# Performance work log

Measured on AMD Instinct MI355X. Metric: run time of the kernel, lower is better.

Reference implementation:

```python
import jax, jax.numpy as jnp
import numpy as np

B, NUM_CLASSES, H, W, CF = 2, 19, 64, 64, 256
TOPK_IDX = 20  # hard-coded in the torch source: sorted descending value at index 20


def _cosine(x):
    # x: [B, N, D] -> clamped cosine affinity [B, N, N]
    xn = x / (jnp.linalg.norm(x, axis=2, keepdims=True) + 1e-9)
    return jnp.maximum(jnp.einsum('bnd,bmd->bnm', xn, xn), 0.0)


def _conv1x1(x, w, b):
    # x: [B, C, H, W], w: [O, C], b: [O]
    return jnp.einsum('bchw,oc->bohw', x, w) + b[None, :, None, None]


def setup_inputs() -> dict:
    key = jax.random.key(0)
    ks = jax.random.split(key, 12)
    s_c = (2.0 / NUM_CLASSES) ** 0.5  # kaiming fan_in scale for 1x1 conv
    s_f = (2.0 / CF) ** 0.5
    return {
        'pred': jax.random.normal(ks[0], (B, NUM_CLASSES, H, W), jnp.float32),
        'feat': jax.random.normal(ks[1], (B, CF, H, W), jnp.float32),
        'w_cls1': jax.random.normal(ks[2], (NUM_CLASSES, NUM_CLASSES), jnp.float32) * s_c,
        'b_cls1': jnp.zeros((NUM_CLASSES,), jnp.float32),
        'w_cls2': jax.random.normal(ks[3], (NUM_CLASSES, NUM_CLASSES), jnp.float32) * s_c,
        'b_cls2': jnp.zeros((NUM_CLASSES,), jnp.float32),
        'w_pro1': jax.random.normal(ks[4], (CF, CF), jnp.float32) * s_f,
        'b_pro1': jnp.zeros((CF,), jnp.float32),
        'w_pro2': jax.random.normal(ks[5], (CF, CF), jnp.float32) * s_f,
        'b_pro2': jnp.zeros((CF,), jnp.float32),
        'class_weight': jnp.ones((NUM_CLASSES,), jnp.float32),
    }


def reference(pred, feat, w_cls1, b_cls1, w_cls2, b_cls2,
              w_pro1, b_pro1, w_pro2, b_pro2, class_weight):
    bsz, c, h, w = feat.shape
    C = pred.shape[1]
    N = h * w
    feat_flat = feat.reshape(bsz, c, N).transpose(0, 2, 1)  # [B, N, 256]

    # --- no_grad block 1: confidence mask + top-k sparsified cosine affinity ---
    prob = jax.nn.softmax(pred, axis=1)
    p_prob = prob.max(axis=1)      # [B, H, W]
    p_max = prob.argmax(axis=1)    # [B, H, W]
    cwm = class_weight / (class_weight.max() + 1e-10) * 0.95
    mask = ((p_prob >= 0.95) | (p_prob >= cwm[p_max])).astype(jnp.float32)
    mask = jax.lax.stop_gradient(mask.reshape(bsz, N, 1))  # broadcast over classes

    aff1 = _cosine(feat_flat)                                # [B, N, N]
    thr = -jnp.sort(-aff1, axis=-1)[:, :, TOPK_IDX:TOPK_IDX + 1]  # per-row 21st largest
    aff1 = jnp.where(aff1 < thr, 0.0, aff1)
    aff1 = jax.lax.stop_gradient(aff1 + aff1.transpose(0, 2, 1))

    # --- degree-normalized propagation of predictions ---
    pred_flat = pred.reshape(bsz, C, N).transpose(0, 2, 1)   # [B, N, C]
    d1 = (aff1.sum(-1) + 1e-10) ** -0.5                      # D^{-1/2}
    aff1n = d1[:, :, None] * aff1 * d1[:, None, :]           # D^{-1/2} A D^{-1/2}
    p2 = jnp.einsum('bnm,bmc->bnc', aff1n, pred_flat)
    p3 = (0.8 * p2 + 0.2 * pred_flat) * (1.0 - mask) + (0.2 * p2 + 0.8 * pred_flat) * mask
    pred2 = p3.transpose(0, 2, 1).reshape(bsz, C, h, w)
    pred_out = _conv1x1(_conv1x1(pred2, w_cls1, b_cls1), w_cls2, b_cls2)

    # --- no_grad block 2: class-consistency-masked affinity over refined softmax ---
    oh = jax.nn.one_hot(p_max, C, dtype=jnp.float32)         # [B, H, W, C]
    # faithful to torch: permute(0,2,3,1) on the already-[B,H,W,C] one-hot, then flat view
    oh = jnp.transpose(oh, (0, 2, 3, 1)).reshape(bsz, -1, C)
    sp = jax.nn.softmax(pred_out, axis=1).reshape(bsz, C, N).transpose(0, 2, 1)
    aff_f = _cosine(sp)
    aff_f = jnp.where(_cosine(oh) == 0.0, 0.0, aff_f)
    d2 = (aff_f.sum(-1) + 1e-10) ** -0.5
    aff_fn = jax.lax.stop_gradient(d2[:, :, None] * aff_f * d2[:, None, :])

    # --- propagate features and project ---
    new_feat = jnp.einsum('bnm,bmc->bnc', aff_fn, feat_flat)
    new_feat = new_feat.transpose(0, 2, 1).reshape(bsz, c, h, w)
    feat_out = _conv1x1(jax.nn.relu(_conv1x1(new_feat, w_pro1, b_pro1)), w_pro2, b_pro2)
    return pred_out, feat_out
```

## Files before the change

kernel.cpp:

```cpp
#include <hip/hip_runtime.h>

#define NN 4096
#define DD 256
#define CC 19
#define BB 2
#define KSPLIT 4

typedef __attribute__((ext_vector_type(8))) short bf16x8;
typedef _Float16 f16x8 __attribute__((ext_vector_type(8)));
typedef __attribute__((ext_vector_type(4))) float f32x4;

#define GLL16(gp, lp) __builtin_amdgcn_global_load_lds( \
    (const __attribute__((address_space(1))) unsigned int*)(gp), \
    (__attribute__((address_space(3))) unsigned int*)(lp), 16, 0, 0)

__device__ inline unsigned short f2b(float f) {
  unsigned int u = __float_as_uint(f);
  return (unsigned short)((u + 0x7FFFu + ((u >> 16) & 1u)) >> 16);
}
__device__ inline float b2f(unsigned short h) {
  return __uint_as_float(((unsigned int)h) << 16);
}
__device__ inline unsigned int pack2(float a, float b) {
  return (unsigned int)f2b(a) | ((unsigned int)f2b(b) << 16);
}
__device__ inline void split16(float x, unsigned short& h, unsigned short& l) {
  _Float16 hh = (_Float16)x;
  float hf = (float)hh;
  _Float16 ll = (_Float16)((x - hf) * 2048.0f);
  h = *reinterpret_cast<unsigned short*>(&hh);
  l = *reinterpret_cast<unsigned short*>(&ll);
}

__global__ void k_mask_bits(const float* __restrict__ pred, const float* __restrict__ cw,
                            float* __restrict__ maskb, unsigned int* __restrict__ ohbits) {
  int g = blockIdx.x * 256 + threadIdx.x;
  if (g >= BB * NN) return;
  int b = g >> 12, n = g & (NN - 1);
  const float* p = pred + (size_t)b * CC * NN + n;
  float v[CC];
  float mx = -1e30f; int am = 0;
#pragma unroll
  for (int c = 0; c < CC; ++c) {
    float t = p[(size_t)c * NN];
    v[c] = t;
    if (t > mx) { mx = t; am = c; }
  }
  float s = 0.f;
#pragma unroll
  for (int c = 0; c < CC; ++c) s += expf(v[c] - mx);
  float pprob = 1.f / s;
  float cmax = 0.f;
#pragma unroll
  for (int c = 0; c < CC; ++c) cmax = fmaxf(cmax, cw[c]);
  float cwm = cw[am] / (cmax + 1e-10f) * 0.95f;
  maskb[g] = (pprob >= 0.95f || pprob >= cwm) ? 1.f : 0.f;
  int h = n >> 6, w = n & 63;
  int L = w * (CC * 64) + am * 64 + h;
  atomicOr(&ohbits[b * NN + L / CC], 1u << (L % CC));
}

__global__ void k_norm_feat(const float* __restrict__ feat,
                            unsigned short* __restrict__ xh, unsigned short* __restrict__ xl) {
  int g = blockIdx.x * 64 + threadIdx.x;
  int b = g >> 12, n = g & (NN - 1);
  const float* f = feat + (size_t)b * DD * NN + n;
  float s = 0.f;
  for (int d = 0; d < DD; ++d) { float t = f[(size_t)d * NN]; s += t * t; }
  float r = 1.f / (sqrtf(s) + 1e-9f);
  size_t ob = ((size_t)b * NN + n) * DD;
  for (int d = 0; d < DD; d += 4) {
    ushort4 oh, ol;
    split16(f[(size_t)d * NN] * r, oh.x, ol.x);
    split16(f[(size_t)(d + 1) * NN] * r, oh.y, ol.y);
    split16(f[(size_t)(d + 2) * NN] * r, oh.z, ol.z);
    split16(f[(size_t)(d + 3) * NN] * r, oh.w, ol.w);
    *reinterpret_cast<ushort4*>(&xh[ob + d]) = oh;
    *reinterpret_cast<ushort4*>(&xl[ob + d]) = ol;
  }
}

__global__ __launch_bounds__(256, 2) void k_gram1(const unsigned short* __restrict__ xh,
                                                  const unsigned short* __restrict__ xl,
                                                  float* __restrict__ M) {
  int L = blockIdx.x;
  int b = blockIdx.y;
  int I = 0;
  while (L >= 32 - I) { L -= 32 - I; ++I; }
  int J = I + L;
  int i0 = I * 128, j0 = J * 128;
  float* Mb = M + (size_t)b * NN * NN;
  const unsigned short* XH = xh + (size_t)b * NN * DD;
  const unsigned short* XL = xl + (size_t)b * NN * DD;
  __shared__ unsigned short stage[2][4][128][32];
  int t = threadIdx.x;
  int wave = t >> 6, lane = t & 63;
  int wr = (wave & 1) * 64, wc = (wave >> 1) * 64;
  int lrow = lane & 15, quad = lane >> 4;
  int sel = (lrow >> 1) & 3;
  f32x4 accH[4][4] = {}, accL[4][4] = {};
  const unsigned short* src = (wave == 0) ? XH + (size_t)i0 * DD
                             : (wave == 1) ? XL + (size_t)i0 * DD
                             : (wave == 2) ? XH + (size_t)j0 * DD
                                           : XL + (size_t)j0 * DD;
  int srow = lane >> 2;
  int spart = (lane & 3) ^ ((lane >> 3) & 3);
#pragma unroll
  for (int e = 0; e < 8; ++e)
    GLL16(&src[(size_t)(e * 16 + srow) * DD + spart * 8], &stage[0][wave][e * 16][0]);
  __syncthreads();
  int cur = 0;
  for (int k0 = 0; k0 < DD; k0 += 32) {
    if (k0 + 32 < DD) {
#pragma unroll
      for (int e = 0; e < 8; ++e)
        GLL16(&src[(size_t)(e * 16 + srow) * DD + k0 + 32 + spart * 8],
              &stage[cur ^ 1][wave][e * 16][0]);
    }
    f16x8 ah[4], al[4], bh[4], bl[4];
#pragma unroll
    for (int i = 0; i < 4; ++i) {
      int ra = wr + i * 16 + lrow;
      int rb = wc + i * 16 + lrow;
      int sl = (quad ^ sel) * 8;
      ah[i] = *reinterpret_cast<const f16x8*>(&stage[cur][0][ra][sl]);
      al[i] = *reinterpret_cast<const f16x8*>(&stage[cur][1][ra][sl]);
      bh[i] = *reinterpret_cast<const f16x8*>(&stage[cur][2][rb][sl]);
      bl[i] = *reinterpret_cast<const f16x8*>(&stage[cur][3][rb][sl]);
    }
#pragma unroll
    for (int i = 0; i < 4; ++i) {
#pragma unroll
      for (int j = 0; j < 4; ++j) {
        accH[i][j] = __builtin_amdgcn_mfma_f32_16x16x32_f16(ah[i], bh[j], accH[i][j], 0, 0, 0);
        accL[i][j] = __builtin_amdgcn_mfma_f32_16x16x32_f16(ah[i], bl[j], accL[i][j], 0, 0, 0);
        accL[i][j] = __builtin_amdgcn_mfma_f32_16x16x32_f16(al[i], bh[j], accL[i][j], 0, 0, 0);
      }
    }
    __syncthreads();
    cur ^= 1;
  }
#pragma unroll
  for (int i = 0; i < 4; ++i)
#pragma unroll
    for (int j = 0; j < 4; ++j)
#pragma unroll
      for (int reg = 0; reg < 4; ++reg)
        accH[i][j][reg] = fmaxf(accH[i][j][reg] + accL[i][j][reg] * 4.8828125e-4f, 0.f);
  float* buf = (float*)stage;
  int rr = t >> 4, cc = t & 15;
  for (int half = 0; half < 2; ++half) {
    __syncthreads();
    if ((wr >> 6) == half) {
#pragma unroll
      for (int i = 0; i < 4; ++i)
#pragma unroll
        for (int j = 0; j < 4; ++j)
#pragma unroll
          for (int reg = 0; reg < 4; ++reg)
            buf[(i * 16 + quad * 4 + reg) * 132 + wc + j * 16 + lrow] = accH[i][j][reg];
    }
    __syncthreads();
#pragma unroll
    for (int i = 0; i < 4; ++i) {
      int row = rr + i * 16;
#pragma unroll
      for (int q = 0; q < 2; ++q) {
        int col = cc * 4 + q * 64;
        *reinterpret_cast<float4*>(&Mb[(size_t)(i0 + half * 64 + row) * NN + j0 + col]) =
            *reinterpret_cast<float4*>(&buf[row * 132 + col]);
      }
    }
  }
  if (I != J) {
    for (int half = 0; half < 2; ++half) {
      __syncthreads();
      if ((wc >> 6) == half) {
#pragma unroll
        for (int i = 0; i < 4; ++i)
#pragma unroll
          for (int j = 0; j < 4; ++j)
#pragma unroll
            for (int reg = 0; reg < 4; ++reg)
              buf[(j * 16 + lrow) * 132 + wr + i * 16 + quad * 4 + reg] = accH[i][j][reg];
      }
      __syncthreads();
#pragma unroll
      for (int i = 0; i < 4; ++i) {
        int row = rr + i * 16;
#pragma unroll
        for (int q = 0; q < 2; ++q) {
          int col = cc * 4 + q * 64;
          *reinterpret_cast<float4*>(&Mb[(size_t)(j0 + half * 64 + row) * NN + i0 + col]) =
              *reinterpret_cast<float4*>(&buf[row * 132 + col]);
        }
      }
    }
  }
}

__global__ __launch_bounds__(256, 2) void k_topk(const float* __restrict__ M,
                                                 float* __restrict__ thr) {
  __shared__ unsigned int cbuf[4][64];
  int b = blockIdx.y;
  int wave = threadIdx.x >> 6, lane = threadIdx.x & 63;
  int n = blockIdx.x * 4 + wave;
  const float* row = M + (size_t)b * NN * NN + (size_t)n * NN;
  uint4 v[16];
#pragma unroll
  for (int e = 0; e < 16; ++e) {
    unsigned long long addr = (unsigned long long)(row + lane * 4 + e * 256);
    asm volatile("global_load_dwordx4 %0, %1, off" : "=v"(v[e]) : "v"(addr));
  }
  asm volatile("s_waitcnt vmcnt(0)" ::: "memory");
  __builtin_amdgcn_sched_barrier(0);
  unsigned int mx = 0u;
#pragma unroll
  for (int e = 0; e < 16; ++e) {
    unsigned int a = v[e].x > v[e].y ? v[e].x : v[e].y;
    unsigned int c2 = v[e].z > v[e].w ? v[e].z : v[e].w;
    a = a > c2 ? a : c2;
    mx = mx > a ? mx : a;
  }
  unsigned int lo = 0u, hi = 0x3FC00000u;
  while (lo < hi) {
    unsigned int mid = lo + ((hi - lo + 1) >> 1);
    if (__popcll(__ballot(mx >= mid)) >= 21) lo = mid; else hi = mid - 1;
  }
  unsigned int s = lo;
  unsigned int base = 0;
  unsigned long long ltmask = (1ull << lane) - 1ull;
#pragma unroll
  for (int e = 0; e < 16; ++e) {
#pragma unroll
    for (int q = 0; q < 4; ++q) {
      unsigned int val = (q == 0) ? v[e].x : (q == 1) ? v[e].y : (q == 2) ? v[e].z : v[e].w;
      unsigned long long mk = __ballot(val >= s);
      if (mk) {
        unsigned int pos = base + (unsigned int)__popcll(mk & ltmask);
        if (val >= s && pos < 64u) cbuf[wave][pos] = val;
        base += (unsigned int)__popcll(mk);
      }
    }
  }
  asm volatile("s_waitcnt lgkmcnt(0)" ::: "memory");
  __builtin_amdgcn_sched_barrier(0);
  unsigned int t = s;
  if (base <= 64u) {
    unsigned int cand = (lane < (int)base) ? cbuf[wave][lane] : 0u;
    lo = s; hi = 0x3FC00000u;
    while (lo < hi) {
      unsigned int mid = lo + ((hi - lo + 1) >> 1);
      if (__popcll(__ballot(cand >= mid)) >= 21) lo = mid; else hi = mid - 1;
    }
    t = lo;
  }
  {
    unsigned int t1 = t + 1u;
    int c1 = 0, c2 = 0;
#pragma unroll
    for (int e = 0; e < 16; ++e) {
      c1 += (int)__popcll(__ballot(v[e].x >= t));
      c1 += (int)__popcll(__ballot(v[e].y >= t));
      c1 += (int)__popcll(__ballot(v[e].z >= t));
      c1 += (int)__popcll(__ballot(v[e].w >= t));
      c2 += (int)__popcll(__ballot(v[e].x >= t1));
      c2 += (int)__popcll(__ballot(v[e].y >= t1));
      c2 += (int)__popcll(__ballot(v[e].z >= t1));
      c2 += (int)__popcll(__ballot(v[e].w >= t1));
    }
    if (!(c1 >= 21 && c2 < 21)) {
      lo = 0u; hi = 0x40000000u;
      while (lo < hi) {
        unsigned int mid = lo + ((hi - lo + 1) >> 1);
        int c = 0;
#pragma unroll
        for (int e = 0; e < 16; ++e) {
          c += (int)__popcll(__ballot(v[e].x >= mid));
          c += (int)__popcll(__ballot(v[e].y >= mid));
          c += (int)__popcll(__ballot(v[e].z >= mid));
          c += (int)__popcll(__ballot(v[e].w >= mid));
        }
        if (c >= 21) lo = mid; else hi = mid - 1;
      }
      t = lo;
    }
  }
  if (lane == 0) thr[b * NN + n] = __uint_as_float(t);
}

__global__ __launch_bounds__(256) void k_symm(float* __restrict__ M, const float* __restrict__ thr,
                                              float* __restrict__ dsum) {
  int L = blockIdx.x;
  int b = blockIdx.y;
  int I = 0;
  while (L >= 64 - I) { L -= 64 - I; ++I; }
  int J = I + L;
  float* Mb = M + (size_t)b * NN * NN;
  unsigned short* Mus = (unsigned short*)Mb;
  const float* th = thr + b * NN;
  __shared__ float A[64][65];
  int t = threadIdx.x;
  int i0 = I * 64, j0 = J * 64;
  float areg[16];
#pragma unroll
  for (int e = 0; e < 16; ++e) {
    int lin = t + e * 256;
    int i = lin >> 6, j = lin & 63;
    areg[e] = Mb[(size_t)(i0 + i) * NN + j0 + j];
  }
#pragma unroll
  for (int e = 0; e < 16; ++e) {
    int lin = t + e * 256;
    int i = lin >> 6, j = lin & 63;
    float a = areg[e];
    float v = a * ((a >= th[i0 + i] ? 1.f : 0.f) + (a >= th[j0 + j] ? 1.f : 0.f));
    A[i][j] = v;
  }
  __syncthreads();
  {
    int i = t >> 2, seg = (t & 3) * 16;
    float v[16];
#pragma unroll
    for (int q = 0; q < 4; ++q)
      *reinterpret_cast<float4*>(&v[q * 4]) = *reinterpret_cast<float4*>(&A[i][seg + q * 4]);
    unsigned int pk[8];
#pragma unroll
    for (int q = 0; q < 8; ++q) pk[q] = pack2(v[2 * q], v[2 * q + 1]);
    size_t ub = 2 * (size_t)(i0 + i) * NN + 2 * (size_t)j0 + seg;
    *reinterpret_cast<int4*>(&Mus[ub])     = *reinterpret_cast<int4*>(&pk[0]);
    *reinterpret_cast<int4*>(&Mus[ub + 8]) = *reinterpret_cast<int4*>(&pk[4]);
  }
  if (I != J) {
    int j = t >> 2, seg = (t & 3) * 16;
    float v[16];
#pragma unroll
    for (int e = 0; e < 16; ++e) v[e] = A[seg + e][j];
    unsigned int pk[8];
#pragma unroll
    for (int q = 0; q < 8; ++q) pk[q] = pack2(v[2 * q], v[2 * q + 1]);
    size_t ub = 2 * (size_t)(j0 + j) * NN + 2 * (size_t)i0 + seg;
    *reinterpret_cast<int4*>(&Mus[ub])     = *reinterpret_cast<int4*>(&pk[0]);
    *reinterpret_cast<int4*>(&Mus[ub + 8]) = *reinterpret_cast<int4*>(&pk[4]);
  }
  if (t < 64) {
    float s = 0.f;
#pragma unroll
    for (int j = 0; j < 64; ++j) s += A[t][j];
    atomicAdd(&dsum[b * NN + i0 + t], s);
  } else if (t < 128 && I != J) {
    int j = t - 64;
    float s = 0.f;
#pragma unroll
    for (int i = 0; i < 64; ++i) s += A[i][j];
    atomicAdd(&dsum[b * NN + j0 + j], s);
  }
}

__global__ void k_fin_d(float* __restrict__ d) {
  int g = blockIdx.x * 256 + threadIdx.x;
  if (g < BB * NN) d[g] = 1.f / sqrtf(d[g] + 1e-10f);
}

__global__ void k_make_yb(const float* __restrict__ pred, const float* __restrict__ d1,
                          unsigned short* __restrict__ ybh) {
  int g = blockIdx.x * 256 + threadIdx.x;
  int idx = g * 4;
  int b = idx / (32 * NN);
  int c = (idx / NN) & 31;
  int n = idx & (NN - 1);
  ushort4 o = make_ushort4(0, 0, 0, 0);
  if (c < CC) {
    float4 p = *reinterpret_cast<const float4*>(&pred[((size_t)b * CC + c) * NN + n]);
    const float* dd = d1 + b * NN + n;
    o.x = f2b(p.x * dd[0]); o.y = f2b(p.y * dd[1]);
    o.z = f2b(p.z * dd[2]); o.w = f2b(p.w * dd[3]);
  }
  *reinterpret_cast<ushort4*>(&ybh[idx]) = o;
}

__global__ __launch_bounds__(256) void k_p2_mfma(
    const float* __restrict__ M, const unsigned short* __restrict__ ybh,
    const float* __restrict__ d1, float* __restrict__ p2b) {
  int b = blockIdx.y;
  int n0 = blockIdx.x * 64;
  const unsigned short* Mus = (const unsigned short*)(M + (size_t)b * NN * NN);
  const unsigned short* Y = ybh + (size_t)b * 32 * NN;
  __shared__ unsigned short As[64][72];
  __shared__ unsigned short Ys[32][72];
  int t = threadIdx.x;
  int wave = t >> 6, lane = t & 63;
  int wn = (wave & 1) * 32;
  int wc = (wave >> 1) * 16;
  int lrow = lane & 15, quad = lane >> 4;
  f32x4 acc[2] = {{0.f,0.f,0.f,0.f},{0.f,0.f,0.f,0.f}};
  int sr = t >> 3, scc = (t & 7) * 8;
  for (int m0 = 0; m0 < NN; m0 += 64) {
#pragma unroll
    for (int e = 0; e < 2; ++e) {
      int rr = sr + e * 32;
      *reinterpret_cast<int4*>(&As[rr][scc]) =
          *reinterpret_cast<const int4*>(&Mus[2 * (size_t)(n0 + rr) * NN + 2 * (size_t)m0 + scc]);
    }
    *reinterpret_cast<int4*>(&Ys[sr][scc]) =
        *reinterpret_cast<const int4*>(&Y[(size_t)sr * NN + m0 + scc]);
    __syncthreads();
#pragma unroll
    for (int kc = 0; kc < 2; ++kc) {
      int ko = kc * 32 + quad * 8;
      bf16x8 bfr = *reinterpret_cast<const bf16x8*>(&Ys[wc + lrow][ko]);
#pragma unroll
      for (int i = 0; i < 2; ++i) {
        bf16x8 af = *reinterpret_cast<const bf16x8*>(&As[wn + i * 16 + lrow][ko]);
        acc[i] = __builtin_amdgcn_mfma_f32_16x16x32_bf16(af, bfr, acc[i], 0, 0, 0);
      }
    }
    __syncthreads();
  }
  int c = wc + lrow;
  if (c < CC) {
#pragma unroll
    for (int i = 0; i < 2; ++i) {
#pragma unroll
      for (int reg = 0; reg < 4; ++reg) {
        int n = n0 + wn + i * 16 + quad * 4 + reg;
        p2b[((size_t)b * NN + n) * CC + c] = d1[b * NN + n] * acc[i][reg];
      }
    }
  }
}

__global__ __launch_bounds__(256) void k_pred_head(const float* __restrict__ pred,
    const float* __restrict__ p2b, const float* __restrict__ maskb,
    const float* __restrict__ w1, const float* __restrict__ b1,
    const float* __restrict__ w2, const float* __restrict__ b2,
    float* __restrict__ out, float* __restrict__ spnT) {
  __shared__ float sw1[CC * CC], sw2[CC * CC], sb1[CC], sb2[CC];
  int t = threadIdx.x;
  for (int i = t; i < CC * CC; i += 256) { sw1[i] = w1[i]; sw2[i] = w2[i]; }
  if (t < CC) { sb1[t] = b1[t]; sb2[t] = b2[t]; }
  __syncthreads();
  int g = blockIdx.x * 256 + t;
  int b = g >> 12, n = g & (NN - 1);
  float m = maskb[g];
  float ca = (m > 0.5f) ? 0.2f : 0.8f;
  float cb = (m > 0.5f) ? 0.8f : 0.2f;
  const float* P = pred + (size_t)b * CC * NN + n;
  const float* Q = p2b + (size_t)g * CC;
  float p3[CC];
#pragma unroll
  for (int c = 0; c < CC; ++c) p3[c] = ca * Q[c] + cb * P[(size_t)c * NN];
  float midv[CC];
#pragma unroll
  for (int o = 0; o < CC; ++o) {
    float s = sb1[o];
#pragma unroll
    for (int c = 0; c < CC; ++c) s += sw1[o * CC + c] * p3[c];
    midv[o] = s;
  }
  float ov[CC];
  float mx = -1e30f;
#pragma unroll
  for (int o = 0; o < CC; ++o) {
    float s = sb2[o];
#pragma unroll
    for (int c = 0; c < CC; ++c) s += sw2[o * CC + c] * midv[c];
    ov[o] = s;
    out[(size_t)b * CC * NN + (size_t)o * NN + n] = s;
    mx = fmaxf(mx, s);
  }
  float se = 0.f;
  float e[CC];
#pragma unroll
  for (int o = 0; o < CC; ++o) { e[o] = expf(ov[o] - mx); se += e[o]; }
  float inv = 1.f / se;
  float nrm = 0.f;
#pragma unroll
  for (int o = 0; o < CC; ++o) { float sp = e[o] * inv; e[o] = sp; nrm += sp * sp; }
  float rn = 1.f / (sqrtf(nrm) + 1e-9f);
#pragma unroll
  for (int o = 0; o < CC; ++o) spnT[(size_t)b * CC * NN + (size_t)o * NN + n] = e[o] * rn;
}

__global__ __launch_bounds__(256) void k_gram2(const float* __restrict__ spnT,
    const unsigned int* __restrict__ bits, unsigned short* __restrict__ Mh) {
  int L = blockIdx.x;
  int b = blockIdx.y;
  int I = 0;
  while (L >= 64 - I) { L -= 64 - I; ++I; }
  int J = I + L;
  const float* X = spnT + (size_t)b * CC * NN;
  unsigned short* Mb = Mh + (size_t)b * NN * NN;
  __shared__ float sA[CC][64], sB[CC][64];
  __shared__ unsigned int bI[64], bJ[64];
  __shared__ float tr[64][65];
  int t = threadIdx.x;
  int r = t >> 4, c = t & 15;
  int i0 = I * 64, j0 = J * 64;
  for (int e = t; e < CC * 64; e += 256) {
    int k = e >> 6, col = e & 63;
    sA[k][col] = X[(size_t)k * NN + i0 + col];
    sB[k][col] = X[(size_t)k * NN + j0 + col];
  }
  if (t < 64) bI[t] = bits[b * NN + i0 + t];
  else if (t < 128) bJ[t - 64] = bits[b * NN + j0 + t - 64];
  __syncthreads();
  float acc[4][4] = {};
#pragma unroll
  for (int k = 0; k < CC; ++k) {
    float av[4], bv[4];
#pragma unroll
    for (int i = 0; i < 4; ++i) av[i] = sA[k][r * 4 + i];
#pragma unroll
    for (int j = 0; j < 4; ++j) bv[j] = sB[k][c * 4 + j];
#pragma unroll
    for (int i = 0; i < 4; ++i) {
#pragma unroll
      for (int j = 0; j < 4; ++j) acc[i][j] += av[i] * bv[j];
    }
  }
#pragma unroll
  for (int i = 0; i < 4; ++i) {
#pragma unroll
    for (int j = 0; j < 4; ++j) {
      bool keep = (bI[r * 4 + i] & bJ[c * 4 + j]) != 0u;
      acc[i][j] = keep ? fmaxf(acc[i][j], 0.f) : 0.f;
    }
    ushort4 v;
    v.x = f2b(acc[i][0]); v.y = f2b(acc[i][1]); v.z = f2b(acc[i][2]); v.w = f2b(acc[i][3]);
    *reinterpret_cast<ushort4*>(&Mb[(size_t)(i0 + r * 4 + i) * NN + j0 + c * 4]) = v;
  }
  if (I != J) {
#pragma unroll
    for (int i = 0; i < 4; ++i) {
#pragma unroll
      for (int j = 0; j < 4; ++j) tr[r * 4 + i][c * 4 + j] = acc[i][j];
    }
    __syncthreads();
#pragma unroll
    for (int e = 0; e < 16; ++e) {
      int lin = t + e * 256;
      int jr = lin >> 6, ic = lin & 63;
      Mb[(size_t)(j0 + jr) * NN + i0 + ic] = f2b(tr[ic][jr]);
    }
  }
}

__global__ __launch_bounds__(256) void k_rowsum2h(const unsigned short* __restrict__ Mh,
                                                  float* __restrict__ d2) {
  int b = blockIdx.y, n = blockIdx.x;
  const unsigned short* row = Mh + (size_t)b * NN * NN + (size_t)n * NN;
  int t = threadIdx.x;
  float s = 0.f;
#pragma unroll
  for (int i = 0; i < 8; ++i) {
    unsigned int u = *reinterpret_cast<const unsigned int*>(&row[(i * 256 + t) * 2]);
    s += __uint_as_float(u << 16) + __uint_as_float(u & 0xffff0000u);
  }
  for (int off = 32; off > 0; off >>= 1) s += __shfl_down(s, off);
  __shared__ float p4[4];
  int wid = t >> 6, lane = t & 63;
  if (lane == 0) p4[wid] = s;
  __syncthreads();
  if (t == 0) d2[b * NN + n] = 1.f / sqrtf(p4[0] + p4[1] + p4[2] + p4[3] + 1e-10f);
}

__global__ void k_make_z(const float* __restrict__ feat, const float* __restrict__ d2,
                         unsigned short* __restrict__ zb) {
  int g = blockIdx.x * 256 + threadIdx.x;
  int idx = g * 4;
  int b = idx / (DD * NN);
  int m = idx & (NN - 1);
  float4 f = *reinterpret_cast<const float4*>(&feat[idx]);
  const float* dd = d2 + b * NN + m;
  ushort4 o;
  o.x = f2b(f.x * dd[0]); o.y = f2b(f.y * dd[1]);
  o.z = f2b(f.z * dd[2]); o.w = f2b(f.w * dd[3]);
  *reinterpret_cast<ushort4*>(&zb[idx]) = o;
}

__global__ void k_prep_w(const float* __restrict__ w1, const float* __restrict__ w2,
                         unsigned short* __restrict__ wb1, unsigned short* __restrict__ wb2) {
  int g = blockIdx.x * 256 + threadIdx.x;
  wb1[g] = f2b(w1[g]);
  wb2[g] = f2b(w2[g]);
}

__global__ __launch_bounds__(256, 2) void k_newfeat_mfma(
    const unsigned short* __restrict__ Mh, const unsigned short* __restrict__ zb,
    float* __restrict__ nfp) {
  int zz = blockIdx.z;
  int b = zz / KSPLIT, ks = zz % KSPLIT;
  int nblk = blockIdx.x;
  int dblk = blockIdx.y;
  const int KLEN = NN / KSPLIT;
  const unsigned short* A = zb + (size_t)b * DD * NN + (size_t)(dblk * 64) * NN + ks * KLEN;
  const unsigned short* Bm = Mh + (size_t)b * NN * NN + (size_t)(nblk * 64) * NN + ks * KLEN;
  __shared__ unsigned short As[2][64][64];
  __shared__ unsigned short Bs[2][64][64];
  int t = threadIdx.x;
  int wave = t >> 6, lane = t & 63;
  int wd = (wave & 1) * 32, wn = (wave >> 1) * 32;
  int lrow = lane & 15, quad = lane >> 4;
  f32x4 acc[2][2] = {{{0.f,0.f,0.f,0.f},{0.f,0.f,0.f,0.f}},{{0.f,0.f,0.f,0.f},{0.f,0.f,0.f,0.f}}};
  int lr3 = lane >> 3;
  int srow = wave * 8 + lr3;
  int spart = (lane & 7) ^ lr3;
#pragma unroll
  for (int e = 0; e < 2; ++e) {
    GLL16(&A [(size_t)(e * 32 + srow) * NN + spart * 8], &As[0][e * 32 + wave * 8][0]);
    GLL16(&Bm[(size_t)(e * 32 + srow) * NN + spart * 8], &Bs[0][e * 32 + wave * 8][0]);
  }
  __syncthreads();
  int cur = 0;
  for (int m0 = 0; m0 < KLEN; m0 += 64) {
    if (m0 + 64 < KLEN) {
#pragma unroll
      for (int e = 0; e < 2; ++e) {
        GLL16(&A [(size_t)(e * 32 + srow) * NN + m0 + 64 + spart * 8],
              &As[cur ^ 1][e * 32 + wave * 8][0]);
        GLL16(&Bm[(size_t)(e * 32 + srow) * NN + m0 + 64 + spart * 8],
              &Bs[cur ^ 1][e * 32 + wave * 8][0]);
      }
    }
#pragma unroll
    for (int kc = 0; kc < 2; ++kc) {
      int sl = ((kc * 4 + quad) ^ (lrow & 7)) * 8;
      bf16x8 af[2], bfr[2];
#pragma unroll
      for (int i = 0; i < 2; ++i) {
        af[i]  = *reinterpret_cast<const bf16x8*>(&As[cur][wd + i * 16 + lrow][sl]);
        bfr[i] = *reinterpret_cast<const bf16x8*>(&Bs[cur][wn + i * 16 + lrow][sl]);
      }
#pragma unroll
      for (int i = 0; i < 2; ++i)
#pragma unroll
        for (int j = 0; j < 2; ++j)
          acc[i][j] = __builtin_amdgcn_mfma_f32_16x16x32_bf16(af[i], bfr[j], acc[i][j], 0, 0, 0);
    }
    __syncthreads();
    cur ^= 1;
  }
#pragma unroll
  for (int j = 0; j < 2; ++j) {
    int n = nblk * 64 + wn + j * 16 + lrow;
#pragma unroll
    for (int i = 0; i < 2; ++i) {
      int d = dblk * 64 + wd + i * 16 + quad * 4;
      float4 v = make_float4(acc[i][j].x, acc[i][j].y, acc[i][j].z, acc[i][j].w);
      *reinterpret_cast<float4*>(&nfp[((size_t)zz * NN + n) * DD + d]) = v;
    }
  }
}

__global__ void k_nf_reduce(const float* __restrict__ nfp, const float* __restrict__ d2,
                            unsigned short* __restrict__ nfh) {
  int g = blockIdx.x * 256 + threadIdx.x;
  int idx = g * 4;
  int b = idx / (NN * DD);
  int n = (idx / DD) & (NN - 1);
  size_t base = (size_t)idx + (size_t)b * (KSPLIT - 1) * NN * DD;
  float4 s = make_float4(0.f, 0.f, 0.f, 0.f);
#pragma unroll
  for (int ks = 0; ks < KSPLIT; ++ks) {
    float4 v = *reinterpret_cast<const float4*>(&nfp[base + (size_t)ks * NN * DD]);
    s.x += v.x; s.y += v.y; s.z += v.z; s.w += v.w;
  }
  float sc = d2[b * NN + n];
  ushort4 o;
  o.x = f2b(s.x * sc); o.y = f2b(s.y * sc); o.z = f2b(s.z * sc); o.w = f2b(s.w * sc);
  *reinterpret_cast<ushort4*>(&nfh[idx]) = o;
}

__global__ __launch_bounds__(256) void k_conv1_mfma(
    const unsigned short* __restrict__ nfh, const unsigned short* __restrict__ wb1,
    const float* __restrict__ b1, unsigned short* __restrict__ midh) {
  int b = blockIdx.z;
  int nblk = blockIdx.x;
  int oblk = blockIdx.y;
  int n0 = nblk * 64, o0 = oblk * 64;
  __shared__ unsigned short As[64][72];
  __shared__ unsigned short Bs[64][72];
  int t = threadIdx.x;
  int wave = t >> 6, lane = t & 63;
  int wn = (wave & 1) * 32, wo = (wave >> 1) * 32;
  int lrow = lane & 15, quad = lane >> 4;
  f32x4 acc[2][2] = {{{0.f,0.f,0.f,0.f},{0.f,0.f,0.f,0.f}},{{0.f,0.f,0.f,0.f},{0.f,0.f,0.f,0.f}}};
  int sr = t >> 3, sc = (t & 7) * 8;
  for (int d0 = 0; d0 < DD; d0 += 64) {
#pragma unroll
    for (int e = 0; e < 2; ++e) {
      int rr = sr + e * 32;
      *reinterpret_cast<int4*>(&As[rr][sc]) =
          *reinterpret_cast<const int4*>(&nfh[((size_t)b * NN + n0 + rr) * DD + d0 + sc]);
      *reinterpret_cast<int4*>(&Bs[rr][sc]) =
          *reinterpret_cast<const int4*>(&wb1[(size_t)(o0 + rr) * DD + d0 + sc]);
    }
    __syncthreads();
#pragma unroll
    for (int kc = 0; kc < 2; ++kc) {
      int ko = kc * 32 + quad * 8;
      bf16x8 af[2], bfr[2];
#pragma unroll
      for (int i = 0; i < 2; ++i) {
        af[i]  = *reinterpret_cast<const bf16x8*>(&As[wn + i * 16 + lrow][ko]);
        bfr[i] = *reinterpret_cast<const bf16x8*>(&Bs[wo + i * 16 + lrow][ko]);
      }
#pragma unroll
      for (int i = 0; i < 2; ++i)
#pragma unroll
        for (int j = 0; j < 2; ++j)
          acc[i][j] = __builtin_amdgcn_mfma_f32_16x16x32_bf16(af[i], bfr[j], acc[i][j], 0, 0, 0);
    }
    __syncthreads();
  }
#pragma unroll
  for (int j = 0; j < 2; ++j) {
    int o = o0 + wo + j * 16 + lrow;
    float bias = b1[o];
#pragma unroll
    for (int i = 0; i < 2; ++i) {
      int nb = n0 + wn + i * 16 + quad * 4;
      ushort4 v;
      v.x = f2b(fmaxf(acc[i][j].x + bias, 0.f));
      v.y = f2b(fmaxf(acc[i][j].y + bias, 0.f));
      v.z = f2b(fmaxf(acc[i][j].z + bias, 0.f));
      v.w = f2b(fmaxf(acc[i][j].w + bias, 0.f));
      *reinterpret_cast<ushort4*>(&midh[((size_t)b * DD + o) * NN + nb]) = v;
    }
  }
}

__global__ __launch_bounds__(256) void k_conv2_mfma(
    const unsigned short* __restrict__ midh, const unsigned short* __restrict__ wb2,
    const float* __restrict__ b2, float* __restrict__ outp) {
  int b = blockIdx.z;
  int nblk = blockIdx.x;
  int oblk = blockIdx.y;
  int n0 = nblk * 64, o0 = oblk * 64;
  __shared__ unsigned short As[64][72];
  __shared__ unsigned short Bs[64][72];
  int t = threadIdx.x;
  int wave = t >> 6, lane = t & 63;
  int wn = (wave & 1) * 32, wo = (wave >> 1) * 32;
  int lrow = lane & 15, quad = lane >> 4;
  f32x4 acc[2][2] = {{{0.f,0.f,0.f,0.f},{0.f,0.f,0.f,0.f}},{{0.f,0.f,0.f,0.f},{0.f,0.f,0.f,0.f}}};
  int sr = t >> 3, sc = (t & 7) * 8;
  for (int d0 = 0; d0 < DD; d0 += 64) {
#pragma unroll
    for (int e = 0; e < 2; ++e) {
      int rr = sr + e * 32;
      *reinterpret_cast<int4*>(&Bs[rr][sc]) =
          *reinterpret_cast<const int4*>(&wb2[(size_t)(o0 + rr) * DD + d0 + sc]);
      unsigned short v[8];
      *reinterpret_cast<int4*>(v) =
          *reinterpret_cast<const int4*>(&midh[((size_t)b * DD + d0 + rr) * NN + n0 + sc]);
#pragma unroll
      for (int j = 0; j < 8; ++j) As[sc + j][rr] = v[j];
    }
    __syncthreads();
#pragma unroll
    for (int kc = 0; kc < 2; ++kc) {
      int ko = kc * 32 + quad * 8;
      bf16x8 af[2], bfr[2];
#pragma unroll
      for (int i = 0; i < 2; ++i) {
        af[i]  = *reinterpret_cast<const bf16x8*>(&As[wn + i * 16 + lrow][ko]);
        bfr[i] = *reinterpret_cast<const bf16x8*>(&Bs[wo + i * 16 + lrow][ko]);
      }
#pragma unroll
      for (int i = 0; i < 2; ++i)
#pragma unroll
        for (int j = 0; j < 2; ++j)
          acc[i][j] = __builtin_amdgcn_mfma_f32_16x16x32_bf16(af[i], bfr[j], acc[i][j], 0, 0, 0);
    }
    __syncthreads();
  }
#pragma unroll
  for (int j = 0; j < 2; ++j) {
    int o = o0 + wo + j * 16 + lrow;
    float bias = b2[o];
#pragma unroll
    for (int i = 0; i < 2; ++i) {
      int nb = n0 + wn + i * 16 + quad * 4;
      float4 v = make_float4(acc[i][j].x + bias, acc[i][j].y + bias,
                             acc[i][j].z + bias, acc[i][j].w + bias);
      *reinterpret_cast<float4*>(&outp[((size_t)b * DD + o) * NN + nb]) = v;
    }
  }
}

extern "C" void kernel_launch(void* const* d_in, const int* in_sizes, int n_in,
                              void* d_out, int out_size, void* d_ws, size_t ws_size,
                              hipStream_t stream) {
  (void)in_sizes; (void)n_in; (void)out_size; (void)ws_size;
  const float* pred   = (const float*)d_in[0];
  const float* feat   = (const float*)d_in[1];
  const float* w_cls1 = (const float*)d_in[2];
  const float* b_cls1 = (const float*)d_in[3];
  const float* w_cls2 = (const float*)d_in[4];
  const float* b_cls2 = (const float*)d_in[5];
  const float* w_pro1 = (const float*)d_in[6];
  const float* b_pro1 = (const float*)d_in[7];
  const float* w_pro2 = (const float*)d_in[8];
  const float* b_pro2 = (const float*)d_in[9];
  const float* cw     = (const float*)d_in[10];
  float* out = (float*)d_out;

  float* Mbuf = (float*)d_ws;
  float* spnT = Mbuf + (size_t)BB * NN * NN;
  float* p2b  = spnT + (size_t)BB * CC * NN;
  float* thr  = p2b + (size_t)BB * NN * CC;
  float* dsum = thr + BB * NN;
  float* d2s  = dsum + BB * NN;
  float* maskb = d2s + BB * NN;
  unsigned int* ohbits = (unsigned int*)(maskb + BB * NN);
  unsigned short* xh   = (unsigned short*)(ohbits + BB * NN);
  unsigned short* xl   = xh + (size_t)BB * NN * DD;
  unsigned short* nfh  = xl + (size_t)BB * NN * DD;
  unsigned short* midh = nfh + (size_t)BB * NN * DD;
  unsigned short* zb   = midh + (size_t)BB * DD * NN;
  unsigned short* wb1  = zb + (size_t)BB * DD * NN;
  unsigned short* wb2  = wb1 + (size_t)DD * DD;
  unsigned short* ybh  = wb2 + (size_t)DD * DD;
  unsigned short* Mh   = (unsigned short*)Mbuf;
  float* nfp = (float*)(Mh + (size_t)BB * NN * NN);

  hipMemsetAsync(dsum, 0, sizeof(float) * BB * NN, stream);
  hipMemsetAsync(ohbits, 0, sizeof(unsigned int) * BB * NN, stream);

  k_mask_bits<<<BB * NN / 256, 256, 0, stream>>>(pred, cw, maskb, ohbits);
  k_norm_feat<<<BB * NN / 64, 64, 0, stream>>>(feat, xh, xl);
  k_gram1<<<dim3(528, BB), 256, 0, stream>>>(xh, xl, Mbuf);
  k_topk<<<dim3(NN / 4, BB), 256, 0, stream>>>(Mbuf, thr);
  k_symm<<<dim3(2080, BB), 256, 0, stream>>>(Mbuf, thr, dsum);
  k_fin_d<<<BB * NN / 256, 256, 0, stream>>>(dsum);
  k_make_yb<<<BB * 32 * NN / 4 / 256, 256, 0, stream>>>(pred, dsum, ybh);
  k_p2_mfma<<<dim3(NN / 64, BB), 256, 0, stream>>>(Mbuf, ybh, dsum, p2b);
  k_pred_head<<<BB * NN / 256, 256, 0, stream>>>(pred, p2b, maskb, w_cls1, b_cls1,
                                                 w_cls2, b_cls2, out, spnT);
  k_gram2<<<dim3(2080, BB), 256, 0, stream>>>(spnT, ohbits, Mh);
  k_rowsum2h<<<dim3(NN, BB), 256, 0, stream>>>(Mh, d2s);
  k_make_z<<<BB * DD * NN / 4 / 256, 256, 0, stream>>>(feat, d2s, zb);
  k_prep_w<<<DD * DD / 256, 256, 0, stream>>>(w_pro1, w_pro2, wb1, wb2);
  k_newfeat_mfma<<<dim3(64, 4, BB * KSPLIT), 256, 0, stream>>>(Mh, zb, nfp);
  k_nf_reduce<<<BB * NN * DD / 4 / 256, 256, 0, stream>>>(nfp, d2s, nfh);
  k_conv1_mfma<<<dim3(64, 4, BB), 256, 0, stream>>>(nfh, wb1, b_pro1, midh);
  k_conv2_mfma<<<dim3(64, 4, BB), 256, 0, stream>>>(midh, wb2, b_pro2,
                                                    out + (size_t)BB * CC * NN);
}
```

Before: 362.9 us.

## Double-buffer p2 MFMA tiles with async global-to-LDS loads and XOR swizzle

Rewrites the k_p2_mfma main loop to prefetch the next M and Y tiles straight into a second LDS buffer using global_load_lds while the current tile feeds the MFMAs. Padding is replaced by an XOR swizzle to avoid bank conflicts, and one barrier per iteration is removed. The aim is to hide global memory latency in this bandwidth-heavy pass over the affinity matrix. The cost is doubled LDS use and a launch bound hint of 2 blocks per SM.

```diff
diff --git a/kernel.cpp b/kernel.cpp
--- a/kernel.cpp
+++ b/kernel.cpp
@@ -379,43 +379,51 @@
   *reinterpret_cast<ushort4*>(&ybh[idx]) = o;
 }
 
-__global__ __launch_bounds__(256) void k_p2_mfma(
+__global__ __launch_bounds__(256, 2) void k_p2_mfma(
     const float* __restrict__ M, const unsigned short* __restrict__ ybh,
     const float* __restrict__ d1, float* __restrict__ p2b) {
   int b = blockIdx.y;
   int n0 = blockIdx.x * 64;
   const unsigned short* Mus = (const unsigned short*)(M + (size_t)b * NN * NN);
   const unsigned short* Y = ybh + (size_t)b * 32 * NN;
-  __shared__ unsigned short As[64][72];
-  __shared__ unsigned short Ys[32][72];
+  __shared__ unsigned short As2[2][64][64];
+  __shared__ unsigned short Ys2[2][32][64];
   int t = threadIdx.x;
   int wave = t >> 6, lane = t & 63;
   int wn = (wave & 1) * 32;
   int wc = (wave >> 1) * 16;
   int lrow = lane & 15, quad = lane >> 4;
   f32x4 acc[2] = {{0.f,0.f,0.f,0.f},{0.f,0.f,0.f,0.f}};
-  int sr = t >> 3, scc = (t & 7) * 8;
+  int lr3 = lane >> 3;
+  int srow = wave * 8 + lr3;
+  int spart = (lane & 7) ^ lr3;
+#pragma unroll
+  for (int e = 0; e < 2; ++e)
+    GLL16(&Mus[2 * (size_t)(n0 + e * 32 + srow) * NN + spart * 8],
+          &As2[0][e * 32 + wave * 8][0]);
+  GLL16(&Y[(size_t)srow * NN + spart * 8], &Ys2[0][wave * 8][0]);
+  __syncthreads();
+  int cur = 0;
   for (int m0 = 0; m0 < NN; m0 += 64) {
-#pragma unroll
-    for (int e = 0; e < 2; ++e) {
-      int rr = sr + e * 32;
-      *reinterpret_cast<int4*>(&As[rr][scc]) =
-          *reinterpret_cast<const int4*>(&Mus[2 * (size_t)(n0 + rr) * NN + 2 * (size_t)m0 + scc]);
-    }
-    *reinterpret_cast<int4*>(&Ys[sr][scc]) =
-        *reinterpret_cast<const int4*>(&Y[(size_t)sr * NN + m0 + scc]);
-    __syncthreads();
+    if (m0 + 64 < NN) {
+#pragma unroll
+      for (int e = 0; e < 2; ++e)
+        GLL16(&Mus[2 * (size_t)(n0 + e * 32 + srow) * NN + 2 * (size_t)(m0 + 64) + spart * 8],
+              &As2[cur ^ 1][e * 32 + wave * 8][0]);
+      GLL16(&Y[(size_t)srow * NN + m0 + 64 + spart * 8], &Ys2[cur ^ 1][wave * 8][0]);
+    }
 #pragma unroll
     for (int kc = 0; kc < 2; ++kc) {
-      int ko = kc * 32 + quad * 8;
-      bf16x8 bfr = *reinterpret_cast<const bf16x8*>(&Ys[wc + lrow][ko]);
+      int sl = ((kc * 4 + quad) ^ (lrow & 7)) * 8;
+      bf16x8 bfr = *reinterpret_cast<const bf16x8*>(&Ys2[cur][wc + lrow][sl]);
 #pragma unroll
       for (int i = 0; i < 2; ++i) {
-        bf16x8 af = *reinterpret_cast<const bf16x8*>(&As[wn + i * 16 + lrow][ko]);
+        bf16x8 af = *reinterpret_cast<const bf16x8*>(&As2[cur][wn + i * 16 + lrow][sl]);
         acc[i] = __builtin_amdgcn_mfma_f32_16x16x32_bf16(af, bfr, acc[i], 0, 0, 0);
       }
     }
     __syncthreads();
+    cur ^= 1;
   }
   int c = wc + lrow;
   if (c < CC) {
```

After: 365.3 us. About the same (+0.7%).
